# Kernel optimization log

Hardware: AMD Instinct MI355X
Metric: run time of the kernel (lower is better)

## Reference

```python
import jax, jax.numpy as jnp
import numpy as np

# MMoE: E experts, each a 2-layer relu MLP (D->H0->H1); T softmax gates over experts.

def setup_inputs() -> dict:
    B, D, H0, H1, E, T = 16384, 1024, 1024, 512, 8, 2
    key = jax.random.key(0)
    ks = jax.random.split(key, 7)
    def glorot(k, shape, fan_in, fan_out):
        lim = jnp.sqrt(6.0 / (fan_in + fan_out)).astype(jnp.float32)
        return jax.random.uniform(k, shape, jnp.float32, -lim, lim)
    inputs = jax.random.normal(ks[0], (B, D), jnp.float32)
    W0 = glorot(ks[1], (E, D, H0), D, H0)      # expert layer 0 kernels
    b0 = jnp.zeros((E, H0), jnp.float32)
    W1 = glorot(ks[2], (E, H0, H1), H0, H1)    # expert layer 1 kernels
    b1 = jnp.zeros((E, H1), jnp.float32)
    Wg = glorot(ks[3], (T, D, E), D, E)        # gate kernels per task
    bg = jnp.zeros((T, E), jnp.float32)
    return {"inputs": inputs, "W0": W0, "b0": b0, "W1": W1, "b1": b1, "Wg": Wg, "bg": bg}


def reference(inputs, W0, b0, W1, b1, Wg, bg):
    # Experts: batched GEMMs over expert axis e.  h: [E, B, H]
    h = jax.nn.relu(jnp.einsum('bd,edh->ebh', inputs, W0) + b0[:, None, :])
    expert_out = jax.nn.relu(jnp.einsum('ebh,ehk->ebk', h, W1) + b1[:, None, :])  # [E, B, H1]
    # Gates: softmax over experts per task.  g: [T, B, E]
    gates = jax.nn.softmax(jnp.einsum('bd,tde->tbe', inputs, Wg) + bg[:, None, :], axis=-1)
    # Gate-weighted sum of expert outputs (einsum 'ai,ian->an' per task)
    outs = jnp.einsum('tbe,ebk->tbk', gates, expert_out)  # [T, B, H1]
    return tuple(outs[t] for t in range(outs.shape[0]))
```

## Files before the change

kernel.cpp:

```cpp
#include <hip/hip_runtime.h>

#define Bsz 16384
#define Dd  1024
#define H0d 1024
#define H1d 512
#define Ee  8
#define Tt  2

typedef short  s8_t  __attribute__((ext_vector_type(8)));
typedef float  fx4   __attribute__((ext_vector_type(4)));
typedef __bf16 bf8_t __attribute__((ext_vector_type(8)));

__device__ __forceinline__ ushort f2bf(float f) {
    uint u = __builtin_bit_cast(uint, f);
    uint r = u + 0x7fffu + ((u >> 16) & 1u);
    return (ushort)(r >> 16);
}
__device__ __forceinline__ float bf2f(ushort u) {
    uint x = ((uint)u) << 16;
    return __builtin_bit_cast(float, x);
}
__device__ __forceinline__ void gload16(const void* g, void* l) {
    __builtin_amdgcn_global_load_lds((const __attribute__((address_space(1))) uint*)g,
                                     (__attribute__((address_space(3))) uint*)l, 16, 0, 0);
}
__device__ __forceinline__ bf8_t ldbf8(const ushort* p) {
    s8_t v = *(const s8_t*)p;
    return __builtin_bit_cast(bf8_t, v);
}

__global__ __launch_bounds__(256) void cvt_bf16_vec(const float* __restrict__ X,
                                                    ushort* __restrict__ Y, int n8) {
    int i = blockIdx.x * 256 + threadIdx.x;
    if (i >= n8) return;
    const float4* p = (const float4*)X + (size_t)i * 2;
    float4 a = p[0], b = p[1];
    s8_t o;
    o[0] = (short)f2bf(a.x); o[1] = (short)f2bf(a.y); o[2] = (short)f2bf(a.z); o[3] = (short)f2bf(a.w);
    o[4] = (short)f2bf(b.x); o[5] = (short)f2bf(b.y); o[6] = (short)f2bf(b.z); o[7] = (short)f2bf(b.w);
    ((s8_t*)Y)[i] = o;
}

__global__ __launch_bounds__(256) void transpose_cvt(const float* __restrict__ W,
                                                     ushort* __restrict__ WT, int R, int Cc) {
    __shared__ float tile[32][33];
    int e = blockIdx.z;
    int r0 = blockIdx.x * 32, c0 = blockIdx.y * 32;
    const float* Wp = W  + (size_t)e * R * Cc;
    ushort*      Tp = WT + (size_t)e * R * Cc;
    int tx = threadIdx.x, ty = threadIdx.y;
    #pragma unroll
    for (int i = 0; i < 32; i += 8)
        tile[ty + i][tx] = Wp[(size_t)(r0 + ty + i) * Cc + c0 + tx];
    __syncthreads();
    #pragma unroll
    for (int i = 0; i < 32; i += 8)
        Tp[(size_t)(c0 + ty + i) * R + r0 + tx] = f2bf(tile[tx][ty + i]);
}

__global__ __launch_bounds__(256) void transpose_wg(const float* __restrict__ Wg,
                                                    ushort* __restrict__ WgT) {
    int i = blockIdx.x * 256 + threadIdx.x;
    int d = i & 1023, r = i >> 10;
    int t = r >> 3, e = r & 7;
    WgT[i] = f2bf(Wg[((size_t)t * 1024 + d) * 8 + e]);
}

__global__ __launch_bounds__(256) void gates_mfma(const ushort* __restrict__ Xb,
                                                  const ushort* __restrict__ WgT,
                                                  const float* __restrict__ bg,
                                                  float* __restrict__ gts) {
    int wave = threadIdx.x >> 6, lane = threadIdx.x & 63;
    int base = blockIdx.x * 64 + wave * 16;
    int l15 = lane & 15, lhi = lane >> 4;
    fx4 acc0 = {}, acc1 = {};
    const ushort* xp = Xb  + (size_t)(base + l15) * Dd + lhi * 8;
    const ushort* wp = WgT + (size_t)l15 * Dd + lhi * 8;
    #pragma unroll
    for (int kt = 0; kt < 32; kt += 2) {
        bf8_t a0 = ldbf8(xp + kt * 32);
        bf8_t b0 = ldbf8(wp + kt * 32);
        bf8_t a1 = ldbf8(xp + kt * 32 + 32);
        bf8_t b1 = ldbf8(wp + kt * 32 + 32);
        acc0 = __builtin_amdgcn_mfma_f32_16x16x32_bf16(a0, b0, acc0, 0, 0, 0);
        acc1 = __builtin_amdgcn_mfma_f32_16x16x32_bf16(a1, b1, acc1, 0, 0, 0);
    }
    fx4 acc = acc0 + acc1;
    float bgv = bg[l15];
    int t = l15 >> 3, e = l15 & 7;
    #pragma unroll
    for (int r = 0; r < 4; ++r) {
        float v = acc[r] + bgv;
        float mx = v;
        mx = fmaxf(mx, __shfl_xor(mx, 1));
        mx = fmaxf(mx, __shfl_xor(mx, 2));
        mx = fmaxf(mx, __shfl_xor(mx, 4));
        float p = expf(v - mx);
        float s = p;
        s += __shfl_xor(s, 1); s += __shfl_xor(s, 2); s += __shfl_xor(s, 4);
        int row = base + lhi * 4 + r;
        gts[(size_t)t * Bsz * 8 + (size_t)row * 8 + e] = p / s;
    }
}

__global__ __launch_bounds__(1024, 4) void gemm256(
    const ushort* __restrict__ A, const ushort* __restrict__ Bt,
    const float* __restrict__ bias, ushort* __restrict__ C,
    int N, int K, int nbn) {
    __shared__ ushort lds[65536];
    char* ldsc = (char*)lds;

    const int tid = threadIdx.x;
    const int wave = tid >> 6, lane = tid & 63;
    const int l15 = lane & 15, lhi = lane >> 4;
    const int wr = wave >> 2, wc = wave & 3;

    int nwg = gridDim.x, wg = blockIdx.x;
    int q = nwg >> 3;
    int swz = (wg & 7) * q + (wg >> 3);
    const int bm = (swz / nbn) * 256, bn = (swz % nbn) * 256;

    const int srcslot = (lane & 7) ^ (lane >> 3);
    const ushort* aSrc = A  + (size_t)(bm + wave * 8 + (lane >> 3)) * K + srcslot * 8;
    const ushort* bSrc = Bt + (size_t)(bn + wave * 8 + (lane >> 3)) * K + srcslot * 8;
    const int sc0 = lhi ^ (l15 & 7);
    const int sc1 = (4 | lhi) ^ (l15 & 7);

    fx4 acc[4][4] = {};

    const int nK = K >> 6;

#define STAGE(KT, d)                                                                            \
    {                                                                                           \
        gload16(aSrc + (size_t)(KT)*64,                ldsc + ((d)*32768 + wave * 1024));       \
        gload16(aSrc + (size_t)128 * K + (size_t)(KT)*64,                                       \
                ldsc + ((d)*32768 + 16384 + wave * 1024));                                      \
        gload16(bSrc + (size_t)(KT)*64,                ldsc + (65536 + (d)*32768 + wave * 1024));\
        gload16(bSrc + (size_t)128 * K + (size_t)(KT)*64,                                       \
                ldsc + (65536 + (d)*32768 + 16384 + wave * 1024));                              \
    }

    STAGE(0, 0);
    __syncthreads();

    for (int kt = 0; kt < nK; ++kt) {
        const int cur = kt & 1;
        if (kt + 1 < nK) STAGE(kt + 1, cur ^ 1);
        bf8_t aF[4][2], bF[4][2];
        #pragma unroll
        for (int m = 0; m < 4; ++m) {
            int Rb = cur * 32768 + (wr * 64 + m * 16 + l15) * 128;
            aF[m][0] = ldbf8((const ushort*)(ldsc + Rb + sc0 * 16));
            aF[m][1] = ldbf8((const ushort*)(ldsc + Rb + sc1 * 16));
        }
        #pragma unroll
        for (int n = 0; n < 4; ++n) {
            int Rb = 65536 + cur * 32768 + (wc * 64 + n * 16 + l15) * 128;
            bF[n][0] = ldbf8((const ushort*)(ldsc + Rb + sc0 * 16));
            bF[n][1] = ldbf8((const ushort*)(ldsc + Rb + sc1 * 16));
        }
        #pragma unroll
        for (int m = 0; m < 4; ++m)
            #pragma unroll
            for (int n = 0; n < 4; ++n)
                #pragma unroll
                for (int kk = 0; kk < 2; ++kk)
                    acc[m][n] = __builtin_amdgcn_mfma_f32_16x16x32_bf16(
                        aF[m][kk], bF[n][kk], acc[m][n], 0, 0, 0);
        __syncthreads();
    }
#undef STAGE

    float bv[4];
    #pragma unroll
    for (int ni = 0; ni < 4; ++ni) bv[ni] = bias[bn + wc * 64 + ni * 16 + l15];
    #pragma unroll
    for (int mi = 0; mi < 4; ++mi) {
        #pragma unroll
        for (int rr = 0; rr < 4; ++rr) {
            int row = bm + wr * 64 + mi * 16 + lhi * 4 + rr;
            ushort* cp = C + (size_t)row * N + bn + wc * 64 + l15;
            #pragma unroll
            for (int ni = 0; ni < 4; ++ni) {
                float v = acc[mi][ni][rr] + bv[ni];
                v = fmaxf(v, 0.f);
                cp[ni * 16] = f2bf(v);
            }
        }
    }
}

template <int MODE>
__global__ __launch_bounds__(256, 2) void gemm_bt(
    const ushort* __restrict__ A, const ushort* __restrict__ Bt,
    const float* __restrict__ bias, ushort* __restrict__ C,
    float* __restrict__ outAcc, const float* __restrict__ gts,
    int expert, int N, int K, int nbn) {
    __shared__ ushort Ash[128 * 64];
    __shared__ ushort Bsh[128 * 64];
    const int tid = threadIdx.x;
    const int wave = tid >> 6, lane = tid & 63;

    int nwg = gridDim.x, wg = blockIdx.x;
    int q = nwg >> 3;
    int swz = (wg & 7) * q + (wg >> 3);
    const int bm = (swz / nbn) * 128, bn = (swz % nbn) * 128;

    const int wm = (wave >> 1) * 64, wn = (wave & 1) * 64;
    const int l15 = lane & 15, lhi = lane >> 4;

    fx4 acc[4][4] = {};

    const int nK = K >> 6;
    for (int kt = 0; kt < nK; ++kt) {
        __syncthreads();
        #pragma unroll
        for (int i = 0; i < 4; ++i) {
            int c = (wave * 4 + i) * 64 + lane;
            int row = c >> 3, g = c & 7;
            const ushort* ga = A + (size_t)(bm + row) * K + kt * 64 + g * 8;
            gload16(ga, (char*)Ash + (wave * 4 + i) * 1024);
            const ushort* gb = Bt + (size_t)(bn + row) * K + kt * 64 + g * 8;
            gload16(gb, (char*)Bsh + (wave * 4 + i) * 1024);
        }
        __syncthreads();
        #pragma unroll
        for (int kk = 0; kk < 2; ++kk) {
            bf8_t af[4], bf_[4];
            #pragma unroll
            for (int m = 0; m < 4; ++m)
                af[m] = ldbf8((const ushort*)((const char*)Ash + (wm + m * 16 + l15) * 128 + kk * 64 + lhi * 16));
            #pragma unroll
            for (int n = 0; n < 4; ++n)
                bf_[n] = ldbf8((const ushort*)((const char*)Bsh + (wn + n * 16 + l15) * 128 + kk * 64 + lhi * 16));
            #pragma unroll
            for (int m = 0; m < 4; ++m)
                #pragma unroll
                for (int n = 0; n < 4; ++n)
                    acc[m][n] = __builtin_amdgcn_mfma_f32_16x16x32_bf16(af[m], bf_[n], acc[m][n], 0, 0, 0);
        }
    }

    #pragma unroll
    for (int m = 0; m < 4; ++m) {
        #pragma unroll
        for (int r = 0; r < 4; ++r) {
            int row = bm + wm + m * 16 + lhi * 4 + r;
            if (MODE == 0) {
                ushort* cp = C + (size_t)row * N + bn + wn + l15;
                #pragma unroll
                for (int n = 0; n < 4; ++n) {
                    float v = acc[m][n][r] + bias[bn + wn + n * 16 + l15];
                    v = fmaxf(v, 0.f);
                    cp[n * 16] = f2bf(v);
                }
            } else {
                float g0 = gts[(size_t)row * 8 + expert];
                float g1 = gts[(size_t)Bsz * 8 + (size_t)row * 8 + expert];
                #pragma unroll
                for (int n = 0; n < 4; ++n) {
                    int col = bn + wn + n * 16 + l15;
                    float v = acc[m][n][r] + bias[col];
                    v = fmaxf(v, 0.f);
                    float* o0 = outAcc + (size_t)row * N + col;
                    float* o1 = outAcc + (size_t)Bsz * N + (size_t)row * N + col;
                    *o0 += g0 * v;
                    *o1 += g1 * v;
                }
            }
        }
    }
}

__global__ __launch_bounds__(256) void combine_kernel(const ushort* __restrict__ eo,
                                                      const float* __restrict__ gts,
                                                      float* __restrict__ out) {
    int wave = threadIdx.x >> 6, lane = threadIdx.x & 63;
    int b = blockIdx.x * 4 + wave;
    float g0[8], g1[8];
    #pragma unroll
    for (int e = 0; e < 8; ++e) {
        g0[e] = gts[(size_t)b * 8 + e];
        g1[e] = gts[(size_t)Bsz * 8 + (size_t)b * 8 + e];
    }
    int k0 = lane * 8;
    float a0[8], a1[8];
    #pragma unroll
    for (int j = 0; j < 8; ++j) { a0[j] = 0.f; a1[j] = 0.f; }
    #pragma unroll
    for (int e = 0; e < 8; ++e) {
        s8_t v = *(const s8_t*)(eo + ((size_t)e * Bsz + b) * H1d + k0);
        #pragma unroll
        for (int j = 0; j < 8; ++j) {
            float f = bf2f((ushort)v[j]);
            a0[j] += g0[e] * f;
            a1[j] += g1[e] * f;
        }
    }
    float4* o0 = (float4*)(out + (size_t)b * H1d + k0);
    o0[0] = make_float4(a0[0], a0[1], a0[2], a0[3]);
    o0[1] = make_float4(a0[4], a0[5], a0[6], a0[7]);
    float4* o1 = (float4*)(out + (size_t)Bsz * H1d + (size_t)b * H1d + k0);
    o1[0] = make_float4(a1[0], a1[1], a1[2], a1[3]);
    o1[1] = make_float4(a1[4], a1[5], a1[6], a1[7]);
}

extern "C" void kernel_launch(void* const* d_in, const int* in_sizes, int n_in,
                              void* d_out, int out_size, void* d_ws, size_t ws_size,
                              hipStream_t stream) {
    const float* X  = (const float*)d_in[0];
    const float* W0 = (const float*)d_in[1];
    const float* b0 = (const float*)d_in[2];
    const float* W1 = (const float*)d_in[3];
    const float* b1 = (const float*)d_in[4];
    const float* Wg = (const float*)d_in[5];
    const float* bg = (const float*)d_in[6];
    float* out = (float*)d_out;

    size_t off = 0;
    auto alloc = [&](size_t bytes) {
        char* p = (char*)d_ws + off;
        off += (bytes + 255) & ~(size_t)255;
        return (void*)p;
    };
    ushort* Xb  = (ushort*)alloc((size_t)Bsz * Dd * 2);
    ushort* W0T = (ushort*)alloc((size_t)Ee * Dd * H0d * 2);
    ushort* W1T = (ushort*)alloc((size_t)Ee * H0d * H1d * 2);
    ushort* h   = (ushort*)alloc((size_t)Bsz * H0d * 2);
    float*  gts = (float*)alloc((size_t)Tt * Bsz * Ee * 4);
    ushort* WgT = (ushort*)alloc((size_t)Tt * Ee * Dd * 2);
    size_t eoBytes = (size_t)Ee * Bsz * H1d * 2;
    bool use_eo = (off + eoBytes) <= ws_size;
    ushort* eo = use_eo ? (ushort*)alloc(eoBytes) : nullptr;

    cvt_bf16_vec<<<(Bsz * Dd / 8 + 255) / 256, 256, 0, stream>>>(X, Xb, Bsz * Dd / 8);
    transpose_cvt<<<dim3(Dd / 32, H0d / 32, Ee), dim3(32, 8), 0, stream>>>(W0, W0T, Dd, H0d);
    transpose_cvt<<<dim3(H0d / 32, H1d / 32, Ee), dim3(32, 8), 0, stream>>>(W1, W1T, H0d, H1d);
    transpose_wg<<<(Tt * Ee * Dd) / 256, 256, 0, stream>>>(Wg, WgT);
    gates_mfma<<<Bsz / 64, 256, 0, stream>>>(Xb, WgT, bg, gts);
    if (!use_eo) hipMemsetAsync(d_out, 0, (size_t)out_size * sizeof(float), stream);

    for (int e = 0; e < Ee; ++e) {
        gemm256<<<dim3((Bsz / 256) * (H0d / 256)), 1024, 0, stream>>>(
            Xb, W0T + (size_t)e * Dd * H0d, b0 + (size_t)e * H0d, h, H0d, Dd, H0d / 256);
        if (use_eo)
            gemm_bt<0><<<dim3((Bsz / 128) * (H1d / 128)), 256, 0, stream>>>(
                h, W1T + (size_t)e * H0d * H1d, b1 + (size_t)e * H1d,
                eo + (size_t)e * Bsz * H1d, nullptr, nullptr, e, H1d, H0d, H1d / 128);
        else
            gemm_bt<1><<<dim3((Bsz / 128) * (H1d / 128)), 256, 0, stream>>>(
                h, W1T + (size_t)e * H0d * H1d, b1 + (size_t)e * H1d,
                nullptr, out, gts, e, H1d, H0d, H1d / 128);
    }
    if (use_eo) combine_kernel<<<Bsz / 4, 256, 0, stream>>>(eo, gts, out);
}
```

Baseline: 578.7 us.

## Batch expert GEMMs across grid y and use 256-tile kernel for second layer

Launches the per-expert GEMMs for groups of up to 8 experts in a single kernel via blockIdx.y, giving each expert its own hidden buffer. The second-layer GEMM now uses the large 256x256 tile kernel instead of the 128x128 one. This cuts the number of launches and fills more of the GPU per launch, at the cost of a larger workspace for hidden activations. The weight-transpose kernel is also vectorized with float4 loads and ushort4 stores.

Measured after the change: 484.6 us (median of 3 runs). 1.19x faster.

```diff
diff --git a/kernel.cpp b/kernel.cpp
--- a/kernel.cpp
+++ b/kernel.cpp
@@ -49,13 +49,16 @@
     const float* Wp = W  + (size_t)e * R * Cc;
     ushort*      Tp = WT + (size_t)e * R * Cc;
     int tx = threadIdx.x, ty = threadIdx.y;
-    #pragma unroll
-    for (int i = 0; i < 32; i += 8)
-        tile[ty + i][tx] = Wp[(size_t)(r0 + ty + i) * Cc + c0 + tx];
+    float4 v = *(const float4*)&Wp[(size_t)(r0 + ty) * Cc + c0 + tx * 4];
+    tile[ty][tx * 4 + 0] = v.x; tile[ty][tx * 4 + 1] = v.y;
+    tile[ty][tx * 4 + 2] = v.z; tile[ty][tx * 4 + 3] = v.w;
     __syncthreads();
-    #pragma unroll
-    for (int i = 0; i < 32; i += 8)
-        Tp[(size_t)(c0 + ty + i) * R + r0 + tx] = f2bf(tile[tx][ty + i]);
+    ushort4 o;
+    o.x = f2bf(tile[tx * 4 + 0][ty]);
+    o.y = f2bf(tile[tx * 4 + 1][ty]);
+    o.z = f2bf(tile[tx * 4 + 2][ty]);
+    o.w = f2bf(tile[tx * 4 + 3][ty]);
+    *(ushort4*)&Tp[(size_t)(c0 + ty) * R + r0 + tx * 4] = o;
 }
 
 __global__ __launch_bounds__(256) void transpose_wg(const float* __restrict__ Wg,
@@ -104,9 +107,9 @@
 }
 
 __global__ __launch_bounds__(1024, 4) void gemm256(
-    const ushort* __restrict__ A, const ushort* __restrict__ Bt,
-    const float* __restrict__ bias, ushort* __restrict__ C,
-    int N, int K, int nbn) {
+    const ushort* __restrict__ Abase, const ushort* __restrict__ BtBase,
+    const float* __restrict__ biasBase, ushort* __restrict__ CBase,
+    int N, int K, int nbn, size_t aStride) {
     __shared__ ushort lds[65536];
     char* ldsc = (char*)lds;
 
@@ -114,6 +117,12 @@
     const int wave = tid >> 6, lane = tid & 63;
     const int l15 = lane & 15, lhi = lane >> 4;
     const int wr = wave >> 2, wc = wave & 3;
+
+    const int ey = blockIdx.y;
+    const ushort* A    = Abase   + (size_t)ey * aStride;
+    const ushort* Bt   = BtBase  + (size_t)ey * (size_t)N * K;
+    const float*  bias = biasBase + (size_t)ey * N;
+    ushort*       C    = CBase   + (size_t)ey * (size_t)Bsz * N;
 
     int nwg = gridDim.x, wg = blockIdx.x;
     int q = nwg >> 3;
@@ -326,31 +335,46 @@
     ushort* Xb  = (ushort*)alloc((size_t)Bsz * Dd * 2);
     ushort* W0T = (ushort*)alloc((size_t)Ee * Dd * H0d * 2);
     ushort* W1T = (ushort*)alloc((size_t)Ee * H0d * H1d * 2);
-    ushort* h   = (ushort*)alloc((size_t)Bsz * H0d * 2);
     float*  gts = (float*)alloc((size_t)Tt * Bsz * Ee * 4);
     ushort* WgT = (ushort*)alloc((size_t)Tt * Ee * Dd * 2);
     size_t eoBytes = (size_t)Ee * Bsz * H1d * 2;
-    bool use_eo = (off + eoBytes) <= ws_size;
+    size_t hBytes  = (size_t)Bsz * H0d * 2;
+    bool use_eo = (off + eoBytes + hBytes + 512) <= ws_size;
     ushort* eo = use_eo ? (ushort*)alloc(eoBytes) : nullptr;
+    int EB = 1;
+    if (use_eo) {
+        size_t rem = (ws_size > off) ? ws_size - off : 0;
+        if (rem >= 8 * (hBytes + 256)) EB = 8;
+        else if (rem >= 4 * (hBytes + 256)) EB = 4;
+        else if (rem >= 2 * (hBytes + 256)) EB = 2;
+    }
+    ushort* hG = (ushort*)alloc((size_t)EB * hBytes);
 
     cvt_bf16_vec<<<(Bsz * Dd / 8 + 255) / 256, 256, 0, stream>>>(X, Xb, Bsz * Dd / 8);
-    transpose_cvt<<<dim3(Dd / 32, H0d / 32, Ee), dim3(32, 8), 0, stream>>>(W0, W0T, Dd, H0d);
-    transpose_cvt<<<dim3(H0d / 32, H1d / 32, Ee), dim3(32, 8), 0, stream>>>(W1, W1T, H0d, H1d);
+    transpose_cvt<<<dim3(Dd / 32, H0d / 32, Ee), dim3(8, 32), 0, stream>>>(W0, W0T, Dd, H0d);
+    transpose_cvt<<<dim3(H0d / 32, H1d / 32, Ee), dim3(8, 32), 0, stream>>>(W1, W1T, H0d, H1d);
     transpose_wg<<<(Tt * Ee * Dd) / 256, 256, 0, stream>>>(Wg, WgT);
     gates_mfma<<<Bsz / 64, 256, 0, stream>>>(Xb, WgT, bg, gts);
     if (!use_eo) hipMemsetAsync(d_out, 0, (size_t)out_size * sizeof(float), stream);
 
-    for (int e = 0; e < Ee; ++e) {
-        gemm256<<<dim3((Bsz / 256) * (H0d / 256)), 1024, 0, stream>>>(
-            Xb, W0T + (size_t)e * Dd * H0d, b0 + (size_t)e * H0d, h, H0d, Dd, H0d / 256);
-        if (use_eo)
-            gemm_bt<0><<<dim3((Bsz / 128) * (H1d / 128)), 256, 0, stream>>>(
-                h, W1T + (size_t)e * H0d * H1d, b1 + (size_t)e * H1d,
-                eo + (size_t)e * Bsz * H1d, nullptr, nullptr, e, H1d, H0d, H1d / 128);
-        else
+    if (use_eo) {
+        for (int g = 0; g < Ee; g += EB) {
+            gemm256<<<dim3((Bsz / 256) * (H0d / 256), EB), 1024, 0, stream>>>(
+                Xb, W0T + (size_t)g * Dd * H0d, b0 + (size_t)g * H0d, hG,
+                H0d, Dd, H0d / 256, 0);
+            gemm256<<<dim3((Bsz / 256) * (H1d / 256), EB), 1024, 0, stream>>>(
+                hG, W1T + (size_t)g * H0d * H1d, b1 + (size_t)g * H1d,
+                eo + (size_t)g * Bsz * H1d, H1d, H0d, H1d / 256, (size_t)Bsz * H0d);
+        }
+        combine_kernel<<<Bsz / 4, 256, 0, stream>>>(eo, gts, out);
+    } else {
+        for (int e = 0; e < Ee; ++e) {
+            gemm256<<<dim3((Bsz / 256) * (H0d / 256), 1), 1024, 0, stream>>>(
+                Xb, W0T + (size_t)e * Dd * H0d, b0 + (size_t)e * H0d, hG,
+                H0d, Dd, H0d / 256, 0);
             gemm_bt<1><<<dim3((Bsz / 128) * (H1d / 128)), 256, 0, stream>>>(
-                h, W1T + (size_t)e * H0d * H1d, b1 + (size_t)e * H1d,
+                hG, W1T + (size_t)e * H0d * H1d, b1 + (size_t)e * H1d,
                 nullptr, out, gts, e, H1d, H0d, H1d / 128);
-    }
-    if (use_eo) combine_kernel<<<Bsz / 4, 256, 0, stream>>>(eo, gts, out);
-}
+        }
+    }
+}
```
